# Optimization experiments

Hardware: AMD Instinct MI355X
Metric: run time of the kernel (lower is better)

The kernel has to match this reference:

```python
import jax, jax.numpy as jnp
import numpy as np

MAXLEN, BATCH, LATENT = 128, 32, 64
DT = 0.1
NSTEPS = 10  # steps = tf.range(0, 1, delta=DT)
HID = 32


def setup_inputs() -> dict:
    key = jax.random.key(0)
    k1, k2, k3 = jax.random.split(key, 3)
    embeddings = jax.random.normal(k1, (BATCH, MAXLEN, LATENT), dtype=jnp.float32)
    # score model: flatten(xt) ++ time -> Dense(32, relu) -> Dense(latent)
    W1 = jax.random.normal(k2, (MAXLEN * LATENT + 1, HID), dtype=jnp.float32) * 0.01
    b1 = jnp.zeros((HID,), jnp.float32)
    W2 = jax.random.normal(k3, (HID, LATENT), dtype=jnp.float32) * 0.001
    b2 = jnp.zeros((LATENT,), jnp.float32)
    return {"embeddings": embeddings, "W1": W1, "b1": b1, "W2": W2, "b2": b2}


def _score_fn(xt, t, W1, b1, W2, b2):
    # xt: (B', L, D), t: (B', 1) -> score (B', D)
    h = jnp.concatenate([xt.reshape(xt.shape[0], -1), t], axis=-1)
    h = jax.nn.relu(h @ W1 + b1)
    return h @ W2 + b2


def _forward(embeddings, W1, b1, W2, b2):
    L, B, D = MAXLEN, BATCH, LATENT
    idx = jnp.arange(L)
    emb_tr = jnp.transpose(embeddings, (1, 0, 2))                    # (L, B, D)
    # vectorized_masking (include=True): mask[t, j] = j < t
    mask = (idx[None, :] < idx[:, None]).astype(embeddings.dtype)    # (L_t, L_j)
    masked = mask[:, :, None, None] * emb_tr[None]                   # (L, L, B, D)
    score_input = masked.reshape(L, L * B, D).transpose(1, 0, 2)     # (L*B, L, D)
    labels = masked[idx, idx]                                        # (L, B, D) diagonal (zeros by construction)
    flat_pos = jnp.arange(B)[None, :] * L + idx[:, None]             # (L, B): index b*L + i

    def step(carry, xs):
        xt, error = carry
        t_val, key = xs
        t = jnp.full((L * B, 1), 1.0, embeddings.dtype) * t_val
        score = _score_fn(xt, t, W1, b1, W2, b2)                     # (L*B, D)
        snorm = jnp.linalg.norm(score)
        dW = jax.random.normal(key, (L * B, D), dtype=embeddings.dtype) * jnp.sqrt(jnp.asarray(DT, embeddings.dtype))
        dx = 0.5 * score * DT + snorm * dW
        xt_tr = xt.transpose(1, 0, 2)                                # (L, L*B, D)
        # update_slice_by_gather for every step i: xt_tr[i, b*L+i] += dx[b*L+i]
        xt_upd = xt_tr.at[idx[:, None], flat_pos].add(dx[flat_pos])  # (L, L*B, D)
        preds = xt_upd.reshape(L, L, B, D)[idx, idx]                 # gather_diagonal_slices -> (L, B, D)
        error = error + jnp.mean((labels - preds) ** 2, axis=-1)     # (L, B)
        return (xt_upd.transpose(1, 0, 2), error), None

    times = jnp.arange(NSTEPS, dtype=embeddings.dtype) * DT
    keys = jax.random.split(jax.random.key(42), NSTEPS)
    init = (score_input, jnp.zeros((L, B), embeddings.dtype))
    (xt_fin, error), _ = jax.lax.scan(step, init, (times, keys))
    xt = xt_fin.reshape(L, L, B, D)[idx, idx].transpose(1, 0, 2)     # (B, L, D)
    step_loss = jnp.sum(error)
    sequence_loss = jnp.mean(jnp.abs(embeddings - xt))
    return xt, step_loss, sequence_loss


def reference(embeddings, W1, b1, W2, b2):
    return _forward(embeddings, W1, b1, W2, b2)
```

## Files before the change

kernel.cpp:

```cpp
#include <hip/hip_runtime.h>
#include <stdint.h>

#define THREEFRY_PARTITIONABLE 1

#define DEV_HOST __host__ __device__

namespace {
constexpr int kNS = 10;
constexpr int kNB = 128;

constexpr int OFF_SUF   = 0;
constexpr int OFF_STEP  = 262144;
constexpr int OFF_RES   = 282624;
constexpr int OFF_LOSSS = 282784;
}

DEV_HOST inline void tf2x32(uint32_t k0, uint32_t k1, uint32_t x0, uint32_t x1,
                            uint32_t& o0, uint32_t& o1) {
  const uint32_t k2 = k0 ^ k1 ^ 0x1BD11BDAu;
#define TF_R(r) { x0 += x1; x1 = (x1 << (r)) | (x1 >> (32 - (r))); x1 ^= x0; }
  x0 += k0; x1 += k1;
  TF_R(13) TF_R(15) TF_R(26) TF_R(6)
  x0 += k1; x1 += k2 + 1u;
  TF_R(17) TF_R(29) TF_R(16) TF_R(24)
  x0 += k2; x1 += k0 + 2u;
  TF_R(13) TF_R(15) TF_R(26) TF_R(6)
  x0 += k0; x1 += k1 + 3u;
  TF_R(17) TF_R(29) TF_R(16) TF_R(24)
  x0 += k1; x1 += k2 + 4u;
  TF_R(13) TF_R(15) TF_R(26) TF_R(6)
  x0 += k2; x1 += k0 + 5u;
#undef TF_R
  o0 = x0; o1 = x1;
}

__device__ inline uint32_t rand_bits(uint32_t key0, uint32_t key1, uint32_t idx) {
#if THREEFRY_PARTITIONABLE
  uint32_t y0, y1;
  tf2x32(key0, key1, 0u, idx, y0, y1);
  return y0 ^ y1;
#else
  const uint32_t half = 262144u / 2;
  uint32_t y0, y1;
  if (idx < half) { tf2x32(key0, key1, idx, half + idx, y0, y1); return y0; }
  tf2x32(key0, key1, idx - half, idx, y0, y1);
  return y1;
#endif
}

__device__ inline float erfinv_xla(float x) {
  float w = -log1pf(-x * x);
  float p;
  if (w < 5.0f) {
    w = w - 2.5f;
    p = 2.81022636e-08f;
    p = fmaf(p, w, 3.43273939e-07f);
    p = fmaf(p, w, -3.5233877e-06f);
    p = fmaf(p, w, -4.39150654e-06f);
    p = fmaf(p, w, 0.00021858087f);
    p = fmaf(p, w, -0.00125372503f);
    p = fmaf(p, w, -0.00417768164f);
    p = fmaf(p, w, 0.246640727f);
    p = fmaf(p, w, 1.50140941f);
  } else {
    w = sqrtf(w) - 3.0f;
    p = -0.000200214257f;
    p = fmaf(p, w, 0.000100950558f);
    p = fmaf(p, w, 0.00134934322f);
    p = fmaf(p, w, -0.00367342844f);
    p = fmaf(p, w, 0.00573950773f);
    p = fmaf(p, w, -0.0076224613f);
    p = fmaf(p, w, 0.00943887047f);
    p = fmaf(p, w, 1.00167406f);
    p = fmaf(p, w, 2.83297682f);
  }
  return p * x;
}

__device__ inline float bits_to_normal(uint32_t bits) {
  const float lo = -0.99999994039535522f;
  float f = __uint_as_float((bits >> 9) | 0x3f800000u) - 1.0f;
  float u = fmaxf(lo, f * 2.0f + lo);
  return 1.41421356237309515f * erfinv_xla(u);
}

__global__ __launch_bounds__(256) void k_suffix(const float* __restrict__ W1,
                                                float* __restrict__ S) {
  const int p = blockIdx.x * 256 + threadIdx.x;
  if (p >= 2048) return;
  const int d = p >> 5, h = p & 31;
  float acc = 0.0f;
  S[(127 * 64 + d) * 32 + h] = 0.0f;
  for (int j = 126; j >= 0; --j) {
    acc += W1[((j + 1) * 64 + d) * 32 + h];
    S[(j * 64 + d) * 32 + h] = acc;
  }
}

struct FusedParams {
  const float* S;
  const float* emb;
  const float* W1;
  const float* b1;
  const float* W2;
  const float* b2;
  float* out;
  float* step;
  float* res;
  float* lossl;
  uint32_t key0[kNS];
  uint32_t key1[kNS];
};

__global__ __launch_bounds__(256, 1) void k_fused(FusedParams p) {
  __shared__ float u_sh[32][64];
  __shared__ float h_sh[32][32];
  __shared__ float wsum[4];
  __shared__ float wsumB[4];
  __shared__ float snorm_sh;
  const int tid = threadIdx.x;
  const int blk = blockIdx.x;
  const int sl = tid >> 5, c = tid & 31;

  int sid[4], jj[4];
  bool contrib[4];
#pragma unroll
  for (int r = 0; r < 4; ++r) {
    const int m = sl + 8 * r;
    sid[r] = blk + 128 * m;
    jj[r]  = (blk >> 5) + 4 * m;
    contrib[r] = (blk == jj[r]);
  }

  float w1reg[64];
#pragma unroll
  for (int d = 0; d < 64; ++d) w1reg[d] = p.W1[(blk * 64 + d) * 32 + c];
  const float w1t = p.W1[8192 * 32 + c];
  float w2r0[32], w2r1[32];
#pragma unroll
  for (int hh = 0; hh < 32; ++hh) {
    w2r0[hh] = p.W2[hh * 64 + c];
    w2r1[hh] = p.W2[hh * 64 + c + 32];
  }
  const float b2_0 = p.b2[c], b2_1 = p.b2[c + 32];

  float basev[4];
  {
    const float b1c = p.b1[c];
    const int bb = blk & 31;
#pragma unroll
    for (int r = 0; r < 4; ++r) {
      const float* e  = p.emb + (bb * 128 + jj[r]) * 64;
      const float* Sp = p.S + (jj[r] * 64) * 32 + c;
      float acc = b1c;
#pragma unroll 16
      for (int d = 0; d < 64; ++d) acc = fmaf(e[d], Sp[d * 32], acc);
      basev[r] = acc;
    }
  }

  float u0[4] = {0.f, 0.f, 0.f, 0.f}, u1[4] = {0.f, 0.f, 0.f, 0.f};
  float lacc = 0.0f;

  for (int k = 0; k < kNS; ++k) {
    const float tval = (float)k * 0.1f;
    if (k == 0) {
#pragma unroll
      for (int r = 0; r < 4; ++r) h_sh[sl + 8 * r][c] = fmaxf(basev[r], 0.0f);
      __syncthreads();
    } else {
#pragma unroll
      for (int r = 0; r < 4; ++r) {
        const int m = sl + 8 * r;
        u_sh[m][c]      = u0[r];
        u_sh[m][c + 32] = u1[r];
      }
      __syncthreads();
#pragma unroll
      for (int r = 0; r < 4; ++r) {
        const int m = sl + 8 * r;
        float pre = fmaf(tval, w1t, basev[r]);
        const float4* up = (const float4*)u_sh[m];
#pragma unroll
        for (int dq = 0; dq < 16; ++dq) {
          const float4 uv = up[dq];
          pre = fmaf(uv.x, w1reg[dq * 4 + 0], pre);
          pre = fmaf(uv.y, w1reg[dq * 4 + 1], pre);
          pre = fmaf(uv.z, w1reg[dq * 4 + 2], pre);
          pre = fmaf(uv.w, w1reg[dq * 4 + 3], pre);
        }
        h_sh[m][c] = fmaxf(pre, 0.0f);
      }
      __syncthreads();
    }
    float sc0[4], sc1[4];
    float sq = 0.0f;
#pragma unroll
    for (int r = 0; r < 4; ++r) {
      const int m = sl + 8 * r;
      float a0 = b2_0, a1 = b2_1;
      const float4* hp = (const float4*)h_sh[m];
#pragma unroll
      for (int hq = 0; hq < 8; ++hq) {
        const float4 hv = hp[hq];
        a0 = fmaf(hv.x, w2r0[hq * 4 + 0], a0); a1 = fmaf(hv.x, w2r1[hq * 4 + 0], a1);
        a0 = fmaf(hv.y, w2r0[hq * 4 + 1], a0); a1 = fmaf(hv.y, w2r1[hq * 4 + 1], a1);
        a0 = fmaf(hv.z, w2r0[hq * 4 + 2], a0); a1 = fmaf(hv.z, w2r1[hq * 4 + 2], a1);
        a0 = fmaf(hv.w, w2r0[hq * 4 + 3], a0); a1 = fmaf(hv.w, w2r1[hq * 4 + 3], a1);
      }
      sc0[r] = a0; sc1[r] = a1;
      sq = fmaf(a0, a0, fmaf(a1, a1, sq));
    }
#pragma unroll
    for (int o = 32; o > 0; o >>= 1) sq += __shfl_down(sq, o);
    if ((tid & 63) == 0) wsum[tid >> 6] = sq;
    __syncthreads();
    if (tid == 0) {
      const float partial = wsum[0] + wsum[1] + wsum[2] + wsum[3];
      const uint64_t pk = ((uint64_t)(uint32_t)(k + 1) << 32) |
                          (uint64_t)__float_as_uint(partial);
      __hip_atomic_store((uint64_t*)(p.step + ((unsigned)k * 128u + (unsigned)blk) * 16u),
                         pk, __ATOMIC_RELAXED, __HIP_MEMORY_SCOPE_AGENT);
    }
    float n0[4], n1[4];
#pragma unroll
    for (int r = 0; r < 4; ++r) {
      const uint32_t e0 = (uint32_t)(sid[r] * 64 + c);
      n0[r] = bits_to_normal(rand_bits(p.key0[k], p.key1[k], e0));
      n1[r] = bits_to_normal(rand_bits(p.key0[k], p.key1[k], e0 + 32u));
    }
    if (blk == 0) {
      if (tid < 64) {
        const unsigned tag = (unsigned)(k + 1);
        const uint64_t* s0p = (const uint64_t*)(p.step + ((unsigned)k * 128u + (unsigned)tid) * 16u);
        const uint64_t* s1p = (const uint64_t*)(p.step + ((unsigned)k * 128u + 64u + (unsigned)tid) * 16u);
        uint64_t v0, v1;
        for (;;) {
          v0 = __hip_atomic_load(s0p, __ATOMIC_RELAXED, __HIP_MEMORY_SCOPE_AGENT);
          v1 = __hip_atomic_load(s1p, __ATOMIC_RELAXED, __HIP_MEMORY_SCOPE_AGENT);
          if (__all(((unsigned)(v0 >> 32) == tag) && ((unsigned)(v1 >> 32) == tag))) break;
          __builtin_amdgcn_s_sleep(1);
        }
        float sum = __uint_as_float((unsigned)(v0 & 0xffffffffu)) +
                    __uint_as_float((unsigned)(v1 & 0xffffffffu));
#pragma unroll
        for (int o = 32; o > 0; o >>= 1) sum += __shfl_down(sum, o);
        if (tid == 0) {
          const float sn = sqrtf(sum);
          snorm_sh = sn;
          const uint64_t rv = ((uint64_t)tag << 32) | (uint64_t)__float_as_uint(sn);
          __hip_atomic_store((uint64_t*)(p.res + (unsigned)k * 16u), rv,
                             __ATOMIC_RELAXED, __HIP_MEMORY_SCOPE_AGENT);
        }
      }
      __syncthreads();
    } else {
      if (tid == 0) {
        const unsigned tag = (unsigned)(k + 1);
        const uint64_t* rl = (const uint64_t*)(p.res + (unsigned)k * 16u);
        uint64_t v;
        for (;;) {
          v = __hip_atomic_load(rl, __ATOMIC_RELAXED, __HIP_MEMORY_SCOPE_AGENT);
          if ((unsigned)(v >> 32) == tag) break;
          __builtin_amdgcn_s_sleep(1);
        }
        snorm_sh = __uint_as_float((unsigned)(v & 0xffffffffu));
      }
      __syncthreads();
    }
    const float snorm = snorm_sh;
#pragma unroll
    for (int r = 0; r < 4; ++r) {
      u0[r] += sc0[r] * 0.05f + snorm * (n0[r] * 0.31622776601683794f);
      u1[r] += sc1[r] * 0.05f + snorm * (n1[r] * 0.31622776601683794f);
      if (contrib[r]) lacc = fmaf(u0[r], u0[r], fmaf(u1[r], u1[r], lacc));
    }
  }

  float lsum = 0.0f;
  {
    const int sl_own = blk & 7;
    const int r_own  = (blk & 31) >> 3;
    if (sl == sl_own) {
      float uo0 = u0[0], uo1 = u1[0];
      if (r_own == 1) { uo0 = u0[1]; uo1 = u1[1]; }
      if (r_own == 2) { uo0 = u0[2]; uo1 = u1[2]; }
      if (r_own == 3) { uo0 = u0[3]; uo1 = u1[3]; }
      const int i_own = 4 * (blk & 31) + (blk >> 5);
      const int b_own = blk & 31;
      const int t_own = blk;
      const int g0 = (b_own * 128 + i_own) * 64 + c;
      const float e0 = p.emb[g0], e1 = p.emb[g0 + 32];
      const bool inc = (i_own < t_own);
      const float v0 = (inc ? e0 : 0.0f) + uo0;
      const float v1 = (inc ? e1 : 0.0f) + uo1;
      p.out[g0]      = v0;
      p.out[g0 + 32] = v1;
      lsum += fabsf(e0 - v0) + fabsf(e1 - v1);
    }
  }
#pragma unroll
  for (int rr = 0; rr < 8; ++rr) {
    const int g = blk * 256 + tid + rr * 32768;
    const int d = g & 63, bi = g >> 6, i = bi & 127, b = bi >> 7;
    if (b == (i >> 2)) continue;
    const int m2 = i * 32 + b;
    const int t = m2 & 127;
    float v = 0.0f;
    if (i < t) v = p.emb[((m2 >> 7) * 128 + i) * 64 + d];
    p.out[g] = v;
    lsum += fabsf(p.emb[g] - v);
  }

  float la = lacc * (1.0f / 64.0f);
#pragma unroll
  for (int o = 32; o > 0; o >>= 1) {
    la   += __shfl_down(la, o);
    lsum += __shfl_down(lsum, o);
  }
  if ((tid & 63) == 0) { wsum[tid >> 6] = la; wsumB[tid >> 6] = lsum; }
  __syncthreads();
  if (tid == 0) {
    const float la_v = wsum[0] + wsum[1] + wsum[2] + wsum[3];
    const float ls_v = wsumB[0] + wsumB[1] + wsumB[2] + wsumB[3];
    uint64_t* slot = (uint64_t*)(p.lossl + (unsigned)blk * 16u);
    __hip_atomic_store(slot, ((uint64_t)11u << 32) | (uint64_t)__float_as_uint(la_v),
                       __ATOMIC_RELAXED, __HIP_MEMORY_SCOPE_AGENT);
    __hip_atomic_store(slot + 1, ((uint64_t)11u << 32) | (uint64_t)__float_as_uint(ls_v),
                       __ATOMIC_RELAXED, __HIP_MEMORY_SCOPE_AGENT);
  }
  if (blk == 0 && tid < 64) {
    const uint64_t* sA = (const uint64_t*)(p.lossl + (unsigned)tid * 16u);
    const uint64_t* sB = (const uint64_t*)(p.lossl + (64u + (unsigned)tid) * 16u);
    uint64_t a0, a1, b0, b1;
    for (;;) {
      a0 = __hip_atomic_load(sA,     __ATOMIC_RELAXED, __HIP_MEMORY_SCOPE_AGENT);
      a1 = __hip_atomic_load(sA + 1, __ATOMIC_RELAXED, __HIP_MEMORY_SCOPE_AGENT);
      b0 = __hip_atomic_load(sB,     __ATOMIC_RELAXED, __HIP_MEMORY_SCOPE_AGENT);
      b1 = __hip_atomic_load(sB + 1, __ATOMIC_RELAXED, __HIP_MEMORY_SCOPE_AGENT);
      const bool ok = ((unsigned)(a0 >> 32) == 11u) && ((unsigned)(a1 >> 32) == 11u) &&
                      ((unsigned)(b0 >> 32) == 11u) && ((unsigned)(b1 >> 32) == 11u);
      if (__all(ok)) break;
      __builtin_amdgcn_s_sleep(1);
    }
    float a = __uint_as_float((unsigned)(a0 & 0xffffffffu)) +
              __uint_as_float((unsigned)(b0 & 0xffffffffu));
    float m = __uint_as_float((unsigned)(a1 & 0xffffffffu)) +
              __uint_as_float((unsigned)(b1 & 0xffffffffu));
#pragma unroll
    for (int o = 32; o > 0; o >>= 1) {
      a += __shfl_down(a, o);
      m += __shfl_down(m, o);
    }
    if (tid == 0) {
      p.out[262144] = a;
      p.out[262145] = m * (1.0f / 262144.0f);
    }
  }
}

static void compute_step_keys(uint32_t keys[kNS][2]) {
#if THREEFRY_PARTITIONABLE
  for (int i = 0; i < kNS; ++i) {
    uint32_t y0, y1;
    tf2x32(0u, 42u, 0u, (uint32_t)i, y0, y1);
    keys[i][0] = y0; keys[i][1] = y1;
  }
#else
  uint32_t a[kNS], b[kNS], outw[2 * kNS];
  for (int i = 0; i < kNS; ++i)
    tf2x32(0u, 42u, (uint32_t)i, (uint32_t)(kNS + i), a[i], b[i]);
  for (int i = 0; i < kNS; ++i) { outw[i] = a[i]; outw[kNS + i] = b[i]; }
  for (int i = 0; i < kNS; ++i) { keys[i][0] = outw[2 * i]; keys[i][1] = outw[2 * i + 1]; }
#endif
}

extern "C" void kernel_launch(void* const* d_in, const int* in_sizes, int n_in,
                              void* d_out, int out_size, void* d_ws, size_t ws_size,
                              hipStream_t stream) {
  (void)in_sizes; (void)n_in; (void)out_size; (void)ws_size;
  const float* emb = (const float*)d_in[0];
  const float* W1  = (const float*)d_in[1];
  const float* b1  = (const float*)d_in[2];
  const float* W2  = (const float*)d_in[3];
  const float* b2  = (const float*)d_in[4];
  float* out = (float*)d_out;
  float* ws  = (float*)d_ws;

  float* S     = ws + OFF_SUF;
  float* step  = ws + OFF_STEP;
  float* res   = ws + OFF_RES;
  float* lossl = ws + OFF_LOSSS;

  uint32_t keys[kNS][2];
  compute_step_keys(keys);

  k_suffix<<<8, 256, 0, stream>>>(W1, S);

  FusedParams p;
  p.S = S; p.emb = emb; p.W1 = W1; p.b1 = b1; p.W2 = W2; p.b2 = b2;
  p.out = out; p.step = step; p.res = res; p.lossl = lossl;
  for (int i = 0; i < kNS; ++i) { p.key0[i] = keys[i][0]; p.key1[i] = keys[i][1]; }

  k_fused<<<kNB, 256, 0, stream>>>(p);
}
```

Before: 192.8 us.

## Halve block count to 64 with 512 threads to shrink grid-wide barrier fan-in

Repartitions the fused persistent kernel from 128 blocks of 256 threads to 64 blocks of 512 threads. Each block now owns two W1 row-slices, one per half-block, and the sample-to-row mapping is remapped to match. The goal is to halve the number of blocks taking part in each per-step cross-block norm reduction and the final loss gather, so polling and fan-in latency drop. In exchange each block holds twice the work, with larger shared buffers and heavier per-thread register pressure, and half as many CUs are used.

```diff
diff --git a/kernel.cpp b/kernel.cpp
--- a/kernel.cpp
+++ b/kernel.cpp
@@ -7,12 +7,12 @@
 
 namespace {
 constexpr int kNS = 10;
-constexpr int kNB = 128;
+constexpr int kNB = 64;
 
 constexpr int OFF_SUF   = 0;
 constexpr int OFF_STEP  = 262144;
-constexpr int OFF_RES   = 282624;
-constexpr int OFF_LOSSS = 282784;
+constexpr int OFF_RES   = 272384;
+constexpr int OFF_LOSSS = 272544;
 }
 
 DEV_HOST inline void tf2x32(uint32_t k0, uint32_t k1, uint32_t x0, uint32_t x1,
@@ -112,29 +112,32 @@
   uint32_t key1[kNS];
 };
 
-__global__ __launch_bounds__(256, 1) void k_fused(FusedParams p) {
-  __shared__ float u_sh[32][64];
-  __shared__ float h_sh[32][32];
-  __shared__ float wsum[4];
-  __shared__ float wsumB[4];
+__global__ __launch_bounds__(512, 1) void k_fused(FusedParams p) {
+  __shared__ float u_sh[64][64];
+  __shared__ float h_sh[64][32];
+  __shared__ float wsum[8];
+  __shared__ float wsumB[8];
   __shared__ float snorm_sh;
   const int tid = threadIdx.x;
   const int blk = blockIdx.x;
-  const int sl = tid >> 5, c = tid & 31;
-
-  int sid[4], jj[4];
+  const int par = tid >> 8;
+  const int t8 = tid & 255;
+  const int sl = t8 >> 5, c = t8 & 31;
+  const int jw = blk + 64 * par;
+
+  int sid[4], jj[4], mm[4];
   bool contrib[4];
 #pragma unroll
   for (int r = 0; r < 4; ++r) {
-    const int m = sl + 8 * r;
-    sid[r] = blk + 128 * m;
-    jj[r]  = (blk >> 5) + 4 * m;
-    contrib[r] = (blk == jj[r]);
+    mm[r]  = 2 * (sl + 8 * r) + par;
+    sid[r] = blk + 64 * mm[r];
+    jj[r]  = 2 * mm[r] + (blk >> 5);
+    contrib[r] = (jw == jj[r]);
   }
 
   float w1reg[64];
 #pragma unroll
-  for (int d = 0; d < 64; ++d) w1reg[d] = p.W1[(blk * 64 + d) * 32 + c];
+  for (int d = 0; d < 64; ++d) w1reg[d] = p.W1[(jw * 64 + d) * 32 + c];
   const float w1t = p.W1[8192 * 32 + c];
   float w2r0[32], w2r1[32];
 #pragma unroll
@@ -166,21 +169,19 @@
     const float tval = (float)k * 0.1f;
     if (k == 0) {
 #pragma unroll
-      for (int r = 0; r < 4; ++r) h_sh[sl + 8 * r][c] = fmaxf(basev[r], 0.0f);
+      for (int r = 0; r < 4; ++r) h_sh[mm[r]][c] = fmaxf(basev[r], 0.0f);
       __syncthreads();
     } else {
 #pragma unroll
       for (int r = 0; r < 4; ++r) {
-        const int m = sl + 8 * r;
-        u_sh[m][c]      = u0[r];
-        u_sh[m][c + 32] = u1[r];
+        u_sh[mm[r]][c]      = u0[r];
+        u_sh[mm[r]][c + 32] = u1[r];
       }
       __syncthreads();
 #pragma unroll
       for (int r = 0; r < 4; ++r) {
-        const int m = sl + 8 * r;
         float pre = fmaf(tval, w1t, basev[r]);
-        const float4* up = (const float4*)u_sh[m];
+        const float4* up = (const float4*)u_sh[mm[r]];
 #pragma unroll
         for (int dq = 0; dq < 16; ++dq) {
           const float4 uv = up[dq];
@@ -189,7 +190,7 @@
           pre = fmaf(uv.z, w1reg[dq * 4 + 2], pre);
           pre = fmaf(uv.w, w1reg[dq * 4 + 3], pre);
         }
-        h_sh[m][c] = fmaxf(pre, 0.0f);
+        h_sh[mm[r]][c] = fmaxf(pre, 0.0f);
       }
       __syncthreads();
     }
@@ -197,9 +198,8 @@
     float sq = 0.0f;
 #pragma unroll
     for (int r = 0; r < 4; ++r) {
-      const int m = sl + 8 * r;
       float a0 = b2_0, a1 = b2_1;
-      const float4* hp = (const float4*)h_sh[m];
+      const float4* hp = (const float4*)h_sh[mm[r]];
 #pragma unroll
       for (int hq = 0; hq < 8; ++hq) {
         const float4 hv = hp[hq];
@@ -216,10 +216,12 @@
     if ((tid & 63) == 0) wsum[tid >> 6] = sq;
     __syncthreads();
     if (tid == 0) {
-      const float partial = wsum[0] + wsum[1] + wsum[2] + wsum[3];
+      float partial = 0.0f;
+#pragma unroll
+      for (int w = 0; w < 8; ++w) partial += wsum[w];
       const uint64_t pk = ((uint64_t)(uint32_t)(k + 1) << 32) |
                           (uint64_t)__float_as_uint(partial);
-      __hip_atomic_store((uint64_t*)(p.step + ((unsigned)k * 128u + (unsigned)blk) * 16u),
+      __hip_atomic_store((uint64_t*)(p.step + ((unsigned)k * 64u + (unsigned)blk) * 16u),
                          pk, __ATOMIC_RELAXED, __HIP_MEMORY_SCOPE_AGENT);
     }
     float n0[4], n1[4];
@@ -232,17 +234,14 @@
     if (blk == 0) {
       if (tid < 64) {
         const unsigned tag = (unsigned)(k + 1);
-        const uint64_t* s0p = (const uint64_t*)(p.step + ((unsigned)k * 128u + (unsigned)tid) * 16u);
-        const uint64_t* s1p = (const uint64_t*)(p.step + ((unsigned)k * 128u + 64u + (unsigned)tid) * 16u);
-        uint64_t v0, v1;
+        const uint64_t* sp = (const uint64_t*)(p.step + ((unsigned)k * 64u + (unsigned)tid) * 16u);
+        uint64_t v;
         for (;;) {
-          v0 = __hip_atomic_load(s0p, __ATOMIC_RELAXED, __HIP_MEMORY_SCOPE_AGENT);
-          v1 = __hip_atomic_load(s1p, __ATOMIC_RELAXED, __HIP_MEMORY_SCOPE_AGENT);
-          if (__all(((unsigned)(v0 >> 32) == tag) && ((unsigned)(v1 >> 32) == tag))) break;
+          v = __hip_atomic_load(sp, __ATOMIC_RELAXED, __HIP_MEMORY_SCOPE_AGENT);
+          if (__all((unsigned)(v >> 32) == tag)) break;
           __builtin_amdgcn_s_sleep(1);
         }
-        float sum = __uint_as_float((unsigned)(v0 & 0xffffffffu)) +
-                    __uint_as_float((unsigned)(v1 & 0xffffffffu));
+        float sum = __uint_as_float((unsigned)(v & 0xffffffffu));
 #pragma unroll
         for (int o = 32; o > 0; o >>= 1) sum += __shfl_down(sum, o);
         if (tid == 0) {
@@ -286,9 +285,9 @@
       if (r_own == 1) { uo0 = u0[1]; uo1 = u1[1]; }
       if (r_own == 2) { uo0 = u0[2]; uo1 = u1[2]; }
       if (r_own == 3) { uo0 = u0[3]; uo1 = u1[3]; }
-      const int i_own = 4 * (blk & 31) + (blk >> 5);
+      const int i_own = 4 * (blk & 31) + (blk >> 5) + 2 * par;
       const int b_own = blk & 31;
-      const int t_own = blk;
+      const int t_own = blk + 64 * par;
       const int g0 = (b_own * 128 + i_own) * 64 + c;
       const float e0 = p.emb[g0], e1 = p.emb[g0 + 32];
       const bool inc = (i_own < t_own);
@@ -301,7 +300,7 @@
   }
 #pragma unroll
   for (int rr = 0; rr < 8; ++rr) {
-    const int g = blk * 256 + tid + rr * 32768;
+    const int g = blk * 512 + tid + rr * 32768;
     const int d = g & 63, bi = g >> 6, i = bi & 127, b = bi >> 7;
     if (b == (i >> 2)) continue;
     const int m2 = i * 32 + b;
@@ -321,8 +320,9 @@
   if ((tid & 63) == 0) { wsum[tid >> 6] = la; wsumB[tid >> 6] = lsum; }
   __syncthreads();
   if (tid == 0) {
-    const float la_v = wsum[0] + wsum[1] + wsum[2] + wsum[3];
-    const float ls_v = wsumB[0] + wsumB[1] + wsumB[2] + wsumB[3];
+    float la_v = 0.0f, ls_v = 0.0f;
+#pragma unroll
+    for (int w = 0; w < 8; ++w) { la_v += wsum[w]; ls_v += wsumB[w]; }
     uint64_t* slot = (uint64_t*)(p.lossl + (unsigned)blk * 16u);
     __hip_atomic_store(slot, ((uint64_t)11u << 32) | (uint64_t)__float_as_uint(la_v),
                        __ATOMIC_RELAXED, __HIP_MEMORY_SCOPE_AGENT);
@@ -331,22 +331,15 @@
   }
   if (blk == 0 && tid < 64) {
     const uint64_t* sA = (const uint64_t*)(p.lossl + (unsigned)tid * 16u);
-    const uint64_t* sB = (const uint64_t*)(p.lossl + (64u + (unsigned)tid) * 16u);
-    uint64_t a0, a1, b0, b1;
+    uint64_t a0, a1;
     for (;;) {
       a0 = __hip_atomic_load(sA,     __ATOMIC_RELAXED, __HIP_MEMORY_SCOPE_AGENT);
       a1 = __hip_atomic_load(sA + 1, __ATOMIC_RELAXED, __HIP_MEMORY_SCOPE_AGENT);
-      b0 = __hip_atomic_load(sB,     __ATOMIC_RELAXED, __HIP_MEMORY_SCOPE_AGENT);
-      b1 = __hip_atomic_load(sB + 1, __ATOMIC_RELAXED, __HIP_MEMORY_SCOPE_AGENT);
-      const bool ok = ((unsigned)(a0 >> 32) == 11u) && ((unsigned)(a1 >> 32) == 11u) &&
-                      ((unsigned)(b0 >> 32) == 11u) && ((unsigned)(b1 >> 32) == 11u);
-      if (__all(ok)) break;
+      if (__all(((unsigned)(a0 >> 32) == 11u) && ((unsigned)(a1 >> 32) == 11u))) break;
       __builtin_amdgcn_s_sleep(1);
     }
-    float a = __uint_as_float((unsigned)(a0 & 0xffffffffu)) +
-              __uint_as_float((unsigned)(b0 & 0xffffffffu));
-    float m = __uint_as_float((unsigned)(a1 & 0xffffffffu)) +
-              __uint_as_float((unsigned)(b1 & 0xffffffffu));
+    float a = __uint_as_float((unsigned)(a0 & 0xffffffffu));
+    float m = __uint_as_float((unsigned)(a1 & 0xffffffffu));
 #pragma unroll
     for (int o = 32; o > 0; o >>= 1) {
       a += __shfl_down(a, o);
@@ -402,5 +395,5 @@
   p.out = out; p.step = step; p.res = res; p.lossl = lossl;
   for (int i = 0; i < kNS; ++i) { p.key0[i] = keys[i][0]; p.key1[i] = keys[i][1]; }
 
-  k_fused<<<kNB, 256, 0, stream>>>(p);
-}
+  k_fused<<<kNB, 512, 0, stream>>>(p);
+}
```

New measurement: 301.6 us. +56.4%, slower.

## Split W1 projection of state update into pre-sync score and noise parts

Applied to the files above, without the earlier changes.

The next-step hidden pre-activation is computed incrementally by projecting the score and the noise through W1 separately, using linearity. Both projections run before the cross-block snorm barrier, which leaves only a scalar FMA on the critical path after the barrier. The aim is to hide the 64-wide W1 matvec under the global reduction wait. The cost is an extra shared-memory buffer, a second dot product per row, and a change in float summation order.

```diff
diff --git a/kernel.cpp b/kernel.cpp
--- a/kernel.cpp
+++ b/kernel.cpp
@@ -113,7 +113,8 @@
 };
 
 __global__ __launch_bounds__(256, 1) void k_fused(FusedParams p) {
-  __shared__ float u_sh[32][64];
+  __shared__ float sc_sh[32][64];
+  __shared__ float nz_sh[32][64];
   __shared__ float h_sh[32][32];
   __shared__ float wsum[4];
   __shared__ float wsumB[4];
@@ -160,39 +161,20 @@
   }
 
   float u0[4] = {0.f, 0.f, 0.f, 0.f}, u1[4] = {0.f, 0.f, 0.f, 0.f};
+  float P_u[4] = {0.f, 0.f, 0.f, 0.f};
   float lacc = 0.0f;
 
   for (int k = 0; k < kNS; ++k) {
     const float tval = (float)k * 0.1f;
-    if (k == 0) {
-#pragma unroll
-      for (int r = 0; r < 4; ++r) h_sh[sl + 8 * r][c] = fmaxf(basev[r], 0.0f);
-      __syncthreads();
-    } else {
-#pragma unroll
-      for (int r = 0; r < 4; ++r) {
-        const int m = sl + 8 * r;
-        u_sh[m][c]      = u0[r];
-        u_sh[m][c + 32] = u1[r];
-      }
-      __syncthreads();
-#pragma unroll
-      for (int r = 0; r < 4; ++r) {
-        const int m = sl + 8 * r;
-        float pre = fmaf(tval, w1t, basev[r]);
-        const float4* up = (const float4*)u_sh[m];
-#pragma unroll
-        for (int dq = 0; dq < 16; ++dq) {
-          const float4 uv = up[dq];
-          pre = fmaf(uv.x, w1reg[dq * 4 + 0], pre);
-          pre = fmaf(uv.y, w1reg[dq * 4 + 1], pre);
-          pre = fmaf(uv.z, w1reg[dq * 4 + 2], pre);
-          pre = fmaf(uv.w, w1reg[dq * 4 + 3], pre);
-        }
-        h_sh[m][c] = fmaxf(pre, 0.0f);
-      }
-      __syncthreads();
-    }
+    const bool last = (k == kNS - 1);
+#pragma unroll
+    for (int r = 0; r < 4; ++r) {
+      const int m = sl + 8 * r;
+      const float pre = (k == 0) ? basev[r]
+                                 : fmaf(tval, w1t, basev[r]) + P_u[r];
+      h_sh[m][c] = fmaxf(pre, 0.0f);
+    }
+    __syncthreads();
     float sc0[4], sc1[4];
     float sq = 0.0f;
 #pragma unroll
@@ -228,6 +210,41 @@
       const uint32_t e0 = (uint32_t)(sid[r] * 64 + c);
       n0[r] = bits_to_normal(rand_bits(p.key0[k], p.key1[k], e0));
       n1[r] = bits_to_normal(rand_bits(p.key0[k], p.key1[k], e0 + 32u));
+    }
+#pragma unroll
+    for (int r = 0; r < 4; ++r) {
+      u0[r] = fmaf(sc0[r], 0.05f, u0[r]);
+      u1[r] = fmaf(sc1[r], 0.05f, u1[r]);
+    }
+    float G_n[4] = {0.f, 0.f, 0.f, 0.f};
+    if (!last) {
+#pragma unroll
+      for (int r = 0; r < 4; ++r) {
+        const int m = sl + 8 * r;
+        sc_sh[m][c]      = sc0[r];
+        sc_sh[m][c + 32] = sc1[r];
+        nz_sh[m][c]      = n0[r];
+        nz_sh[m][c + 32] = n1[r];
+      }
+      __syncthreads();
+#pragma unroll
+      for (int r = 0; r < 4; ++r) {
+        const int m = sl + 8 * r;
+        const float4* sp = (const float4*)sc_sh[m];
+        const float4* np = (const float4*)nz_sh[m];
+        float gs = 0.f, gn = 0.f;
+#pragma unroll
+        for (int dq = 0; dq < 16; ++dq) {
+          const float4 sv = sp[dq];
+          const float4 nv = np[dq];
+          gs = fmaf(sv.x, w1reg[dq * 4 + 0], gs); gn = fmaf(nv.x, w1reg[dq * 4 + 0], gn);
+          gs = fmaf(sv.y, w1reg[dq * 4 + 1], gs); gn = fmaf(nv.y, w1reg[dq * 4 + 1], gn);
+          gs = fmaf(sv.z, w1reg[dq * 4 + 2], gs); gn = fmaf(nv.z, w1reg[dq * 4 + 2], gn);
+          gs = fmaf(sv.w, w1reg[dq * 4 + 3], gs); gn = fmaf(nv.w, w1reg[dq * 4 + 3], gn);
+        }
+        P_u[r] = fmaf(gs, 0.05f, P_u[r]);
+        G_n[r] = gn;
+      }
     }
     if (blk == 0) {
       if (tid < 64) {
@@ -268,12 +285,16 @@
       }
       __syncthreads();
     }
-    const float snorm = snorm_sh;
-#pragma unroll
-    for (int r = 0; r < 4; ++r) {
-      u0[r] += sc0[r] * 0.05f + snorm * (n0[r] * 0.31622776601683794f);
-      u1[r] += sc1[r] * 0.05f + snorm * (n1[r] * 0.31622776601683794f);
+    const float sns = snorm_sh * 0.31622776601683794f;
+#pragma unroll
+    for (int r = 0; r < 4; ++r) {
+      u0[r] = fmaf(sns, n0[r], u0[r]);
+      u1[r] = fmaf(sns, n1[r], u1[r]);
       if (contrib[r]) lacc = fmaf(u0[r], u0[r], fmaf(u1[r], u1[r], lacc));
+    }
+    if (!last) {
+#pragma unroll
+      for (int r = 0; r < 4; ++r) P_u[r] = fmaf(sns, G_n[r], P_u[r]);
     }
   }
 
```

Result: slower. 280.8 us (+45.7%).
